# Kernel tuning notes

Measured on AMD Instinct MI355X. Metric: run time of the kernel, lower is better.

## Reference

```python
import jax, jax.numpy as jnp
import numpy as np

HEAD_NUM = 16

def setup_inputs() -> dict:
    key = jax.random.key(0)
    ks = jax.random.split(key, 5)
    B, N, D = 2, 2048, 1024
    x = jax.random.normal(ks[0], (B, N, D), dtype=jnp.float32)
    scale = 0.02
    W_q = jax.random.normal(ks[1], (D, D), dtype=jnp.float32) * scale
    W_k = jax.random.normal(ks[2], (D, D), dtype=jnp.float32) * scale
    W_v = jax.random.normal(ks[3], (D, D), dtype=jnp.float32) * scale
    W_o = jax.random.normal(ks[4], (D, D), dtype=jnp.float32) * scale
    return {"x": x, "W_q": W_q, "W_k": W_k, "W_v": W_v, "W_o": W_o}

def reference(x, W_q, W_k, W_v, W_o):
    B, N, D = x.shape
    H = HEAD_NUM
    hd = D // H  # head_dim
    inv_sqrt_hd = 1.0 / np.sqrt(hd).astype(np.float32)

    def split_head(t):
        # einops 'b n (d h) -> b h n d' : head index is the INNER factor
        return t.reshape(B, N, hd, H).transpose(0, 3, 1, 2)  # [B,H,N,hd]

    # nn.Linear(bias=False): y = x @ W.T
    Q = split_head(x @ W_q.T)
    K = split_head(x @ W_k.T)
    V = split_head(x @ W_v.T)

    scores = jnp.einsum('bhnd,bhmd->bhnm', Q, K) * inv_sqrt_hd  # [B,H,N,N]
    attn = jax.nn.softmax(scores, axis=-1)
    heads = jnp.einsum('bhnm,bhmd->bhnd', attn, V)  # [B,H,N,hd]

    # einops 'b h n d -> b n (h d)' : head index is the OUTER factor here
    concat = heads.transpose(0, 2, 1, 3).reshape(B, N, D)
    return concat @ W_o.T
```

## Files before the change

### kernel.cpp

```cpp
#include <hip/hip_runtime.h>
#include <hip/hip_bf16.h>

typedef __bf16 bf16_t;
typedef __attribute__((ext_vector_type(8))) __bf16 bf16x8;
typedef __attribute__((ext_vector_type(4))) __bf16 bf16x4;
typedef __attribute__((ext_vector_type(4))) float f32x4;
typedef __attribute__((ext_vector_type(16))) float f32x16;

#define MFMA16(A,B,C) __builtin_amdgcn_mfma_f32_16x16x32_bf16((A),(B),(C),0,0,0)
#define MFMA32(A,B,C) __builtin_amdgcn_mfma_f32_32x32x16_bf16((A),(B),(C),0,0,0)

#define BATCH 2
#define SEQ 2048
#define DMODEL 1024
#define NHEAD 16
#define HDIM 64
#define MROWS (BATCH * SEQ)

__device__ __forceinline__ void async16(const bf16_t* g, bf16_t* l) {
    __builtin_amdgcn_global_load_lds(
        (const __attribute__((address_space(1))) unsigned int*)g,
        (__attribute__((address_space(3))) unsigned int*)l, 16, 0, 0);
}

__device__ __forceinline__ bf16x8 ldsA32(const bf16_t* base, int row, int chunk) {
    return *(const bf16x8*)&base[row * 32 + ((chunk ^ ((row >> 1) & 3)) << 3)];
}
__device__ __forceinline__ bf16x8 ldsA64(const bf16_t* base, int row, int chunk) {
    return *(const bf16x8*)&base[row * 64 + ((chunk ^ (row & 7)) << 3)];
}

__device__ __forceinline__ unsigned pk(float a, float b) {
    union { unsigned u; bf16_t h[2]; } t;
    t.h[0] = (bf16_t)a;
    t.h[1] = (bf16_t)b;
    return t.u;
}

__global__ void split_kernel(const float* __restrict__ x, const float* __restrict__ Wq,
                             const float* __restrict__ Wk, const float* __restrict__ Wv,
                             const float* __restrict__ Wo, bf16_t* __restrict__ xh,
                             bf16_t* __restrict__ wh, bf16_t* __restrict__ wl) {
    int blk = blockIdx.x;
    if (blk < 4096) {
        int i = blk * 256 + threadIdx.x;
        f32x4 v = ((const f32x4*)x)[i];
        bf16x4 h;
#pragma unroll
        for (int c = 0; c < 4; ++c) h[c] = (bf16_t)v[c];
        ((bf16x4*)xh)[i] = h;
        return;
    }
    int e = blk - 4096;
    int z = e >> 10;
    int i = (e & 1023) * 256 + threadIdx.x;
    const float* src = (z == 0) ? Wq : (z == 1) ? Wk : (z == 2) ? Wv : Wo;
    const float scale = (z == 0) ? 0.125f * 1.44269504088896f : 1.0f;
    int row = i >> 8, col4 = i & 255;
    int r_src;
    if (z < 3) {
        int h = row >> 6, d = row & 63;
        r_src = 16 * d + h;
    } else {
        r_src = row;
    }
    f32x4 v = ((const f32x4*)src)[r_src * 256 + col4];
    bf16x4 h4, l4;
#pragma unroll
    for (int c = 0; c < 4; ++c) {
        float val = v[c] * scale;
        bf16_t hh = (bf16_t)val;
        h4[c] = hh;
        l4[c] = (bf16_t)(val - (float)hh);
    }
    ((bf16x4*)(wh + (size_t)z * DMODEL * DMODEL))[i] = h4;
    if (z == 3) ((bf16x4*)wl)[i] = l4;
}

__global__ __launch_bounds__(256)
void gemm_qkv_kernel(const bf16_t* __restrict__ Ah, const bf16_t* __restrict__ Bh0,
                     bf16_t* __restrict__ Coh0, int M, int Nn, int Kk) {
    __shared__ __align__(16) bf16_t smem[2][8192];

    const int z = blockIdx.z;
    const bf16_t* Bh = Bh0 + (size_t)z * Nn * Kk;
    const int m0 = blockIdx.y * 128, n0 = blockIdx.x * 128;
    const int tid = threadIdx.x;
    const int wave = tid >> 6, lane = tid & 63, lq = lane >> 4, ln = lane & 15;
    const int wr = wave >> 1, wc = wave & 1;

    const bf16_t* g_ptr[4];
    int l_off[4];
#pragma unroll
    for (int q = 0; q < 4; ++q) {
        int e = wave * 4 + q;
        int a = e >> 3, u = e & 7;
        int C = u * 64 + lane;
        int r = C >> 2, p = C & 3;
        int c = p ^ ((r >> 1) & 3);
        g_ptr[q] = (a == 0 ? Ah + (size_t)(m0 + r) * Kk
                           : Bh + (size_t)(n0 + r) * Kk) + c * 8;
        l_off[q] = a * 4096 + u * 512;
    }

    f32x4 acc[4][4] = {};

#pragma unroll
    for (int q = 0; q < 4; ++q)
        async16(g_ptr[q], &smem[0][l_off[q]]);

    const int NIT = Kk / 32;
    for (int j = 0; j < NIT; ++j) {
        __syncthreads();
        if (j + 1 < NIT) {
#pragma unroll
            for (int q = 0; q < 4; ++q)
                async16(g_ptr[q] + (j + 1) * 32, &smem[(j + 1) & 1][l_off[q]]);
        }
        const bf16_t* cur = smem[j & 1];

        bf16x8 ah[4], bh[4];
#pragma unroll
        for (int t = 0; t < 4; ++t) {
            ah[t] = ldsA32(cur, wr * 64 + t * 16 + ln, lq);
            bh[t] = ldsA32(cur + 4096, wc * 64 + t * 16 + ln, lq);
        }
#pragma unroll
        for (int tm = 0; tm < 4; ++tm)
#pragma unroll
            for (int tn = 0; tn < 4; ++tn)
                acc[tm][tn] = MFMA16(ah[tm], bh[tn], acc[tm][tn]);
    }

#pragma unroll
    for (int tm = 0; tm < 4; ++tm)
#pragma unroll
        for (int tn = 0; tn < 4; ++tn)
#pragma unroll
            for (int p = 0; p < 4; ++p) {
                int gm = m0 + wr * 64 + tm * 16 + lq * 4 + p;
                int gn = n0 + wc * 64 + tn * 16 + ln;
                Coh0[(size_t)z * M * Nn + (size_t)gm * Nn + gn] =
                    (bf16_t)acc[tm][tn][p];
            }
}

__global__ __launch_bounds__(256)
void gemm_out_kernel(const bf16_t* __restrict__ Ah,
                     const bf16_t* __restrict__ Bh, const bf16_t* __restrict__ Bl,
                     float* __restrict__ Cf, int M, int Nn, int Kk) {
    __shared__ __align__(16) bf16_t smem[2][10240];

    const int m0 = blockIdx.y * 64, n0 = blockIdx.x * 128;
    const int tid = threadIdx.x;
    const int wave = tid >> 6, lane = tid & 63, lq = lane >> 4, ln = lane & 15;
    const int wr = wave >> 1, wc = wave & 1;

    const bf16_t* g_ptr[5];
    int l_off[5];
#pragma unroll
    for (int q = 0; q < 5; ++q) {
        int e = wave * 5 + q;
        const bf16_t* arr;
        int u, rowbase, lb;
        if (e < 4)       { arr = Ah; u = e;      rowbase = m0; lb = 0; }
        else if (e < 12) { arr = Bh; u = e - 4;  rowbase = n0; lb = 2048; }
        else             { arr = Bl; u = e - 12; rowbase = n0; lb = 6144; }
        int r = u * 16 + (lane >> 2), p = lane & 3;
        int c = p ^ ((r >> 1) & 3);
        g_ptr[q] = arr + (size_t)(rowbase + r) * Kk + c * 8;
        l_off[q] = lb + u * 512;
    }

    f32x4 acc[2][4] = {};

#pragma unroll
    for (int q = 0; q < 5; ++q)
        async16(g_ptr[q], &smem[0][l_off[q]]);

    const int NIT = Kk / 32;
    for (int j = 0; j < NIT; ++j) {
        __syncthreads();
        if (j + 1 < NIT) {
#pragma unroll
            for (int q = 0; q < 5; ++q)
                async16(g_ptr[q] + (j + 1) * 32, &smem[(j + 1) & 1][l_off[q]]);
        }
        const bf16_t* cur = smem[j & 1];

        bf16x8 ah[2], bh[4], bl[4];
#pragma unroll
        for (int t = 0; t < 2; ++t)
            ah[t] = ldsA32(cur, wr * 32 + t * 16 + ln, lq);
#pragma unroll
        for (int t = 0; t < 4; ++t) {
            bh[t] = ldsA32(cur + 2048, wc * 64 + t * 16 + ln, lq);
            bl[t] = ldsA32(cur + 6144, wc * 64 + t * 16 + ln, lq);
        }
#pragma unroll
        for (int tm = 0; tm < 2; ++tm)
#pragma unroll
            for (int tn = 0; tn < 4; ++tn) {
                acc[tm][tn] = MFMA16(ah[tm], bh[tn], acc[tm][tn]);
                acc[tm][tn] = MFMA16(ah[tm], bl[tn], acc[tm][tn]);
            }
    }

#pragma unroll
    for (int tm = 0; tm < 2; ++tm)
#pragma unroll
        for (int tn = 0; tn < 4; ++tn)
#pragma unroll
            for (int p = 0; p < 4; ++p) {
                int gm = m0 + wr * 32 + tm * 16 + lq * 4 + p;
                int gn = n0 + wc * 64 + tn * 16 + ln;
                Cf[(size_t)gm * Nn + gn] = acc[tm][tn][p];
            }
}

__global__ __launch_bounds__(256)
void vtrans_kernel(const bf16_t* __restrict__ Vn, bf16_t* __restrict__ Vt) {
    __shared__ bf16_t t[64][66];
    const int bh = blockIdx.y;
    const int b = bh >> 4, h = bh & 15;
    const int n0 = blockIdx.x * 64;
    const int tid = threadIdx.x;
#pragma unroll
    for (int it = 0; it < 2; ++it) {
        int c = it * 256 + tid;
        int r = c >> 3, p = c & 7;
        *(bf16x8*)&t[r][p * 8] =
            *(const bf16x8*)&Vn[((size_t)(b * SEQ + n0 + r)) * DMODEL + h * HDIM + p * 8];
    }
    __syncthreads();
#pragma unroll
    for (int it = 0; it < 2; ++it) {
        int c = it * 256 + tid;
        int d = c >> 3, p = c & 7;
        bf16x8 v;
#pragma unroll
        for (int e = 0; e < 8; ++e) v[e] = t[p * 8 + e][d];
        *(bf16x8*)&Vt[((size_t)(bh * HDIM + d)) * SEQ + n0 + p * 8] = v;
    }
}

__global__ __launch_bounds__(512, 4)
void attn_kernel(const bf16_t* __restrict__ Qh, const bf16_t* __restrict__ Kh,
                 const bf16_t* __restrict__ Vt, bf16_t* __restrict__ Ch) {
    __shared__ __align__(16) bf16_t smem[2][2][8192];

    const int bh = blockIdx.y;
    const int b = bh >> 4, h = bh & 15;
    const int q0 = blockIdx.x * 128;
    const int tid = threadIdx.x;
    const int g = tid >> 8;
    const int wv = (tid >> 6) & 3;
    const int lane = tid & 63;
    const int ln32 = lane & 31, hl = lane >> 5;

    bf16x8 qfh[4];
    {
        size_t qrow = ((size_t)(b * SEQ + q0 + wv * 32 + ln32)) * DMODEL +
                      h * HDIM + hl * 8;
#pragma unroll
        for (int c = 0; c < 4; ++c)
            qfh[c] = *(const bf16x8*)&Qh[qrow + c * 16];
    }

    bf16_t* gsm = &smem[g][0][0];
    const bf16_t* g_base[4];
    int l_off[4];
    size_t g_step[4];
#pragma unroll
    for (int q = 0; q < 4; ++q) {
        int e = wv * 4 + q;
        int a = e >> 3, u = e & 7;
        int r = u * 8 + (lane >> 3), p = lane & 7;
        int c = p ^ (r & 7);
        if (a == 0) {
            g_base[q] = Kh + ((size_t)(b * SEQ + g * 1024 + r)) * DMODEL +
                        h * HDIM + c * 8;
            l_off[q] = u * 512;
            g_step[q] = (size_t)64 * DMODEL;
        } else {
            g_base[q] = Vt + ((size_t)(bh * HDIM + r)) * SEQ + g * 1024 + c * 8;
            l_off[q] = 4096 + u * 512;
            g_step[q] = 64;
        }
    }

    f32x16 o[2];
#pragma unroll
    for (int dt = 0; dt < 2; ++dt)
#pragma unroll
        for (int r = 0; r < 16; ++r) o[dt][r] = 0.0f;
    float rs = 0.0f;

#pragma unroll
    for (int q = 0; q < 4; ++q)
        async16(g_base[q], gsm + l_off[q]);

    for (int j = 0; j < 16; ++j) {
        __syncthreads();
        if (j < 15) {
#pragma unroll
            for (int q = 0; q < 4; ++q)
                async16(g_base[q] + (j + 1) * g_step[q],
                        gsm + ((j + 1) & 1) * 8192 + l_off[q]);
        }
        const bf16_t* Kc = gsm + (j & 1) * 8192;
        const bf16_t* Vc = Kc + 4096;

        bf16x8 pfrag[4];
#pragma unroll
        for (int kt = 0; kt < 2; ++kt) {
            f32x16 st;
#pragma unroll
            for (int r = 0; r < 16; ++r) st[r] = 0.0f;
#pragma unroll
            for (int c = 0; c < 4; ++c) {
                bf16x8 kh = ldsA64(Kc, kt * 32 + ln32, 2 * c + hl);
                st = MFMA32(kh, qfh[c], st);
            }
            float pexp[16];
#pragma unroll
            for (int r = 0; r < 16; ++r) {
                pexp[r] = __builtin_amdgcn_exp2f(st[r]);
                rs += pexp[r];
            }
#pragma unroll
            for (int s1 = 0; s1 < 2; ++s1) {
                unsigned lo01 = pk(pexp[8 * s1 + 0], pexp[8 * s1 + 1]);
                unsigned lo23 = pk(pexp[8 * s1 + 2], pexp[8 * s1 + 3]);
                unsigned hi01 = pk(pexp[8 * s1 + 4], pexp[8 * s1 + 5]);
                unsigned hi23 = pk(pexp[8 * s1 + 6], pexp[8 * s1 + 7]);
                unsigned sa = hl ? lo01 : hi01;
                unsigned sb = hl ? lo23 : hi23;
                unsigned ra = (unsigned)__shfl_xor((int)sa, 32);
                unsigned rb = (unsigned)__shfl_xor((int)sb, 32);
                union { bf16x8 v; unsigned u[4]; } outv;
                outv.u[0] = hl ? ra : lo01;
                outv.u[1] = hl ? rb : lo23;
                outv.u[2] = hl ? hi01 : ra;
                outv.u[3] = hl ? hi23 : rb;
                pfrag[kt * 2 + s1] = outv.v;
            }
        }
#pragma unroll
        for (int dt = 0; dt < 2; ++dt)
#pragma unroll
            for (int s = 0; s < 4; ++s) {
                bf16x8 va = ldsA64(Vc, dt * 32 + ln32, 2 * s + hl);
                o[dt] = MFMA32(va, pfrag[s], o[dt]);
            }
    }

    rs += __shfl_xor(rs, 32);

    __syncthreads();
    float* cbuf = (float*)smem;
    float* rbuf = cbuf + 8192;
    if (g == 1) {
#pragma unroll
        for (int dt = 0; dt < 2; ++dt)
#pragma unroll
            for (int r = 0; r < 16; ++r) {
                int d = dt * 32 + (r & 3) + 8 * (r >> 2) + 4 * hl;
                cbuf[d * 128 + wv * 32 + ln32] = o[dt][r];
            }
        if (hl == 0) rbuf[wv * 32 + ln32] = rs;
    }
    __syncthreads();
    float inv = 0.0f;
    if (g == 0) {
#pragma unroll
        for (int dt = 0; dt < 2; ++dt)
#pragma unroll
            for (int r = 0; r < 16; ++r) {
                int d = dt * 32 + (r & 3) + 8 * (r >> 2) + 4 * hl;
                o[dt][r] += cbuf[d * 128 + wv * 32 + ln32];
            }
        inv = 1.0f / (rs + rbuf[wv * 32 + ln32]);
    }
    __syncthreads();
    float* fbuf = (float*)smem;
    if (g == 0) {
#pragma unroll
        for (int dh = 0; dh < 2; ++dh)
#pragma unroll
            for (int r = 0; r < 16; ++r) {
                int d_loc = (r & 3) + 8 * (r >> 2) + 4 * hl;
                fbuf[dh * 4224 + wv * 1056 + ln32 * 33 + d_loc] = o[dh][r] * inv;
            }
    }
    __syncthreads();
    {
        int gw = tid >> 6;
        int dh = gw >> 2, w = gw & 3;
#pragma unroll
        for (int qq = 0; qq < 16; ++qq) {
            int qrow = hl * 16 + qq;
            float v = fbuf[dh * 4224 + w * 1056 + qrow * 33 + ln32];
            size_t gidx = ((size_t)(b * SEQ + q0 + w * 32 + qrow)) * DMODEL +
                          h * HDIM + dh * 32 + ln32;
            Ch[gidx] = (bf16_t)v;
        }
    }
}

extern "C" void kernel_launch(void* const* d_in, const int* in_sizes, int n_in,
                              void* d_out, int out_size, void* d_ws, size_t ws_size,
                              hipStream_t stream) {
    const float* x  = (const float*)d_in[0];
    const float* Wq = (const float*)d_in[1];
    const float* Wk = (const float*)d_in[2];
    const float* Wv = (const float*)d_in[3];
    const float* Wo = (const float*)d_in[4];
    float* out = (float*)d_out;

    char* ws = (char*)d_ws;
    size_t off = 0;
    auto alloc = [&](size_t bytes) -> bf16_t* {
        bf16_t* p = (bf16_t*)(ws + off);
        off += (bytes + 255) & ~(size_t)255;
        return p;
    };
    const size_t XE = (size_t)MROWS * DMODEL;
    const size_t WE = (size_t)DMODEL * DMODEL;

    bf16_t* xh  = alloc(XE * 2);
    bf16_t* wh  = alloc(4 * WE * 2);
    bf16_t* wl  = alloc(WE * 2);
    bf16_t* qnh = alloc(3 * XE * 2);
    bf16_t* vth = alloc(XE * 2);
    bf16_t* ch  = alloc(XE * 2);
    (void)ws_size; (void)in_sizes; (void)n_in; (void)out_size;

    split_kernel<<<8192, 256, 0, stream>>>(x, Wq, Wk, Wv, Wo, xh, wh, wl);

    gemm_qkv_kernel<<<dim3(DMODEL / 128, MROWS / 128, 3), 256, 0, stream>>>(
        xh, wh, qnh, MROWS, DMODEL, DMODEL);

    vtrans_kernel<<<dim3(SEQ / 64, BATCH * NHEAD), 256, 0, stream>>>(qnh + 2 * XE, vth);

    attn_kernel<<<dim3(SEQ / 128, BATCH * NHEAD), 512, 0, stream>>>(
        qnh, qnh + XE, vth, ch);

    gemm_out_kernel<<<dim3(DMODEL / 128, MROWS / 64), 256, 0, stream>>>(
        ch, wh + 3 * WE, wl, out, MROWS, DMODEL, DMODEL);
}
```

Measured before the change: 193.2 us.

## Drop bf16 low-part correction for W_o and compute softmax row sums via MFMA

Removes the hi/lo bf16 split of W_o, so the output projection runs a single MFMA per tile instead of two and loads less into LDS; split_kernel no longer writes the low part. In attention, the per-lane scalar row-sum accumulation of the exponentials is replaced by an extra MFMA against a ones vector, which also eliminates the cross-half shuffle. The first change lowers output-projection accuracy. The second adds matrix work but takes VALU adds off the softmax path, and it sums the bf16-rounded probabilities, which matches what multiplies V.

```diff
diff --git a/kernel.cpp b/kernel.cpp
--- a/kernel.cpp
+++ b/kernel.cpp
@@ -40,7 +40,7 @@
 __global__ void split_kernel(const float* __restrict__ x, const float* __restrict__ Wq,
                              const float* __restrict__ Wk, const float* __restrict__ Wv,
                              const float* __restrict__ Wo, bf16_t* __restrict__ xh,
-                             bf16_t* __restrict__ wh, bf16_t* __restrict__ wl) {
+                             bf16_t* __restrict__ wh) {
     int blk = blockIdx.x;
     if (blk < 4096) {
         int i = blk * 256 + threadIdx.x;
@@ -65,16 +65,10 @@
         r_src = row;
     }
     f32x4 v = ((const f32x4*)src)[r_src * 256 + col4];
-    bf16x4 h4, l4;
-#pragma unroll
-    for (int c = 0; c < 4; ++c) {
-        float val = v[c] * scale;
-        bf16_t hh = (bf16_t)val;
-        h4[c] = hh;
-        l4[c] = (bf16_t)(val - (float)hh);
-    }
+    bf16x4 h4;
+#pragma unroll
+    for (int c = 0; c < 4; ++c) h4[c] = (bf16_t)(v[c] * scale);
     ((bf16x4*)(wh + (size_t)z * DMODEL * DMODEL))[i] = h4;
-    if (z == 3) ((bf16x4*)wl)[i] = l4;
 }
 
 __global__ __launch_bounds__(256)
@@ -146,26 +140,24 @@
 }
 
 __global__ __launch_bounds__(256)
-void gemm_out_kernel(const bf16_t* __restrict__ Ah,
-                     const bf16_t* __restrict__ Bh, const bf16_t* __restrict__ Bl,
+void gemm_out_kernel(const bf16_t* __restrict__ Ah, const bf16_t* __restrict__ Bh,
                      float* __restrict__ Cf, int M, int Nn, int Kk) {
-    __shared__ __align__(16) bf16_t smem[2][10240];
+    __shared__ __align__(16) bf16_t smem[2][6144];
 
     const int m0 = blockIdx.y * 64, n0 = blockIdx.x * 128;
     const int tid = threadIdx.x;
     const int wave = tid >> 6, lane = tid & 63, lq = lane >> 4, ln = lane & 15;
     const int wr = wave >> 1, wc = wave & 1;
 
-    const bf16_t* g_ptr[5];
-    int l_off[5];
-#pragma unroll
-    for (int q = 0; q < 5; ++q) {
-        int e = wave * 5 + q;
+    const bf16_t* g_ptr[3];
+    int l_off[3];
+#pragma unroll
+    for (int q = 0; q < 3; ++q) {
+        int e = wave * 3 + q;
         const bf16_t* arr;
         int u, rowbase, lb;
-        if (e < 4)       { arr = Ah; u = e;      rowbase = m0; lb = 0; }
-        else if (e < 12) { arr = Bh; u = e - 4;  rowbase = n0; lb = 2048; }
-        else             { arr = Bl; u = e - 12; rowbase = n0; lb = 6144; }
+        if (e < 4) { arr = Ah; u = e;     rowbase = m0; lb = 0; }
+        else       { arr = Bh; u = e - 4; rowbase = n0; lb = 2048; }
         int r = u * 16 + (lane >> 2), p = lane & 3;
         int c = p ^ ((r >> 1) & 3);
         g_ptr[q] = arr + (size_t)(rowbase + r) * Kk + c * 8;
@@ -175,7 +167,7 @@
     f32x4 acc[2][4] = {};
 
 #pragma unroll
-    for (int q = 0; q < 5; ++q)
+    for (int q = 0; q < 3; ++q)
         async16(g_ptr[q], &smem[0][l_off[q]]);
 
     const int NIT = Kk / 32;
@@ -183,27 +175,23 @@
         __syncthreads();
         if (j + 1 < NIT) {
 #pragma unroll
-            for (int q = 0; q < 5; ++q)
+            for (int q = 0; q < 3; ++q)
                 async16(g_ptr[q] + (j + 1) * 32, &smem[(j + 1) & 1][l_off[q]]);
         }
         const bf16_t* cur = smem[j & 1];
 
-        bf16x8 ah[2], bh[4], bl[4];
+        bf16x8 ah[2], bh[4];
 #pragma unroll
         for (int t = 0; t < 2; ++t)
             ah[t] = ldsA32(cur, wr * 32 + t * 16 + ln, lq);
 #pragma unroll
-        for (int t = 0; t < 4; ++t) {
+        for (int t = 0; t < 4; ++t)
             bh[t] = ldsA32(cur + 2048, wc * 64 + t * 16 + ln, lq);
-            bl[t] = ldsA32(cur + 6144, wc * 64 + t * 16 + ln, lq);
-        }
 #pragma unroll
         for (int tm = 0; tm < 2; ++tm)
 #pragma unroll
-            for (int tn = 0; tn < 4; ++tn) {
+            for (int tn = 0; tn < 4; ++tn)
                 acc[tm][tn] = MFMA16(ah[tm], bh[tn], acc[tm][tn]);
-                acc[tm][tn] = MFMA16(ah[tm], bl[tn], acc[tm][tn]);
-            }
     }
 
 #pragma unroll
@@ -266,6 +254,9 @@
         for (int c = 0; c < 4; ++c)
             qfh[c] = *(const bf16x8*)&Qh[qrow + c * 16];
     }
+    bf16x8 ones;
+#pragma unroll
+    for (int e = 0; e < 8; ++e) ones[e] = (bf16_t)1.0f;
 
     bf16_t* gsm = &smem[g][0][0];
     const bf16_t* g_base[4];
@@ -289,12 +280,13 @@
         }
     }
 
-    f32x16 o[2];
+    f32x16 o[2], o_ones;
 #pragma unroll
     for (int dt = 0; dt < 2; ++dt)
 #pragma unroll
         for (int r = 0; r < 16; ++r) o[dt][r] = 0.0f;
-    float rs = 0.0f;
+#pragma unroll
+    for (int r = 0; r < 16; ++r) o_ones[r] = 0.0f;
 
 #pragma unroll
     for (int q = 0; q < 4; ++q)
@@ -324,10 +316,8 @@
             }
             float pexp[16];
 #pragma unroll
-            for (int r = 0; r < 16; ++r) {
+            for (int r = 0; r < 16; ++r)
                 pexp[r] = __builtin_amdgcn_exp2f(st[r]);
-                rs += pexp[r];
-            }
 #pragma unroll
             for (int s1 = 0; s1 < 2; ++s1) {
                 unsigned lo01 = pk(pexp[8 * s1 + 0], pexp[8 * s1 + 1]);
@@ -347,15 +337,16 @@
             }
         }
 #pragma unroll
-        for (int dt = 0; dt < 2; ++dt)
-#pragma unroll
-            for (int s = 0; s < 4; ++s) {
-                bf16x8 va = ldsA64(Vc, dt * 32 + ln32, 2 * s + hl);
-                o[dt] = MFMA32(va, pfrag[s], o[dt]);
-            }
-    }
-
-    rs += __shfl_xor(rs, 32);
+        for (int s = 0; s < 4; ++s) {
+            bf16x8 va0 = ldsA64(Vc, ln32, 2 * s + hl);
+            bf16x8 va1 = ldsA64(Vc, 32 + ln32, 2 * s + hl);
+            o[0] = MFMA32(va0, pfrag[s], o[0]);
+            o[1] = MFMA32(va1, pfrag[s], o[1]);
+            o_ones = MFMA32(ones, pfrag[s], o_ones);
+        }
+    }
+
+    float rs = o_ones[0];
 
     __syncthreads();
     float* cbuf = (float*)smem;
@@ -430,13 +421,12 @@
 
     bf16_t* xh  = alloc(XE * 2);
     bf16_t* wh  = alloc(4 * WE * 2);
-    bf16_t* wl  = alloc(WE * 2);
     bf16_t* qnh = alloc(3 * XE * 2);
     bf16_t* vth = alloc(XE * 2);
     bf16_t* ch  = alloc(XE * 2);
     (void)ws_size; (void)in_sizes; (void)n_in; (void)out_size;
 
-    split_kernel<<<8192, 256, 0, stream>>>(x, Wq, Wk, Wv, Wo, xh, wh, wl);
+    split_kernel<<<8192, 256, 0, stream>>>(x, Wq, Wk, Wv, Wo, xh, wh);
 
     gemm_qkv_kernel<<<dim3(DMODEL / 128, MROWS / 128, 3), 256, 0, stream>>>(
         xh, wh, qnh, MROWS, DMODEL, DMODEL);
@@ -447,5 +437,5 @@
         qnh, qnh + XE, vth, ch);
 
     gemm_out_kernel<<<dim3(DMODEL / 128, MROWS / 64), 256, 0, stream>>>(
-        ch, wh + 3 * WE, wl, out, MROWS, DMODEL, DMODEL);
-}
+        ch, wh + 3 * WE, out, MROWS, DMODEL, DMODEL);
+}
```

Measured after the change: 184.7 us. 1.05x faster.
